# Optimization experiments

Hardware: AMD Instinct MI355X
Metric: run time of the kernel (lower is better)

## Reference

```python
import jax, jax.numpy as jnp
import numpy as np


def setup_inputs() -> dict:
    key = jax.random.key(0)
    k0, k1, k2, k3, k4 = jax.random.split(key, 5)
    Ns, N, D = 1024, 192, 24
    # spins in {-1, +1}
    x = (2.0 * jax.random.randint(k0, (Ns, N), 0, 2) - 1.0).astype(jnp.float32)
    # symmetric distance-index matrix with values in [0, D)
    r = jax.random.randint(k1, (N, N), 0, D)
    nd = jnp.minimum(r, r.T).astype(jnp.int32)
    W2 = 0.1 * jax.random.normal(k2, (D,), dtype=jnp.float32)
    W3 = 0.01 * jax.random.normal(k3, (D, D), dtype=jnp.float32)
    # positive mean-field coefficients so log(phi) is real
    phi = 0.5 + jax.random.uniform(k4, (N, 2), dtype=jnp.float32)
    return {"x": x, "W2": W2, "W3": W3, "phi": phi, "neighbors_distances": nd}


def reference(x, W2, W3, phi, neighbors_distances):
    # x: (Ns, N) spins in {-1,+1}; W2: (D,); W3: (D,D); phi: (N,2); nd: (N,N) int in [0,D)
    nd = neighbors_distances
    N = x.shape[-1]

    # J2[n] = 0.5 * sum_{i,j} x[n,i] * W2[nd[i,j]] * x[n,j]
    J2 = 0.5 * jnp.einsum('ni,ij,nj->n', x, W2[nd], x)

    # J3[n] = sum_{i,j,k} W3[nd[k,j], nd[i,j]] x[n,k] x[n,i] x[n,j]
    G = W3[nd]                                  # (N,N,D): G[k,j,d] = W3[nd[k,j], d]
    S = jnp.einsum('nk,kjd->njd', x, G)         # (Ns,N,D)
    j_idx = jnp.broadcast_to(jnp.arange(N)[None, :], (N, N))
    M = S[:, j_idx, nd]                         # (Ns,N,N): M[n,i,j] = S[n, j, nd[i,j]]
    J3 = jnp.einsum('nij,ni,nj->n', M, x, x)

    # mean-field: sum_i log(phi[i, (1+x[n,i])/2])
    idx = jax.lax.stop_gradient(((1.0 + x) * 0.5)).astype(jnp.int32)  # (Ns,N) in {0,1}
    mf = phi[jnp.arange(N)[None, :], idx]       # (Ns,N)
    logmf = jnp.sum(jnp.log(mf), axis=-1)

    return J2 + J3 + logmf
```

## Files before the change

kernel.cpp:

```cpp
#include <hip/hip_runtime.h>
#include <math.h>


#define NS   1024
#define NN   192
#define DD   24
#define CPAD 25

__global__ __launch_bounds__(NN) void jmf3_kernel(
    const float* __restrict__ x,
    const float* __restrict__ W2,
    const float* __restrict__ W3,
    const float* __restrict__ phi,
    const int*   __restrict__ nd,
    float* __restrict__ out)
{
    __shared__ float sx[NN];
    __shared__ float sW3[DD * DD];
    __shared__ float sW2[DD];
    __shared__ float sc[NN * CPAD];
    __shared__ float red[3];

    const int tid = threadIdx.x;
    const int n   = blockIdx.x;

    sx[tid] = x[n * NN + tid];
    sW3[tid]       = W3[tid];
    sW3[tid + 192] = W3[tid + 192];
    sW3[tid + 384] = W3[tid + 384];
    if (tid < DD) sW2[tid] = W2[tid];
    #pragma unroll
    for (int r = 0; r < CPAD; ++r) sc[tid * CPAD + r] = 0.0f;
    __syncthreads();

    const int j = tid;
    float* cj = &sc[j * CPAD];
    for (int i = 0; i < NN; ++i) {
        int r = nd[i * NN + j];
        cj[r] += sx[i];
    }

    float c[DD];
    #pragma unroll
    for (int r = 0; r < DD; ++r) c[r] = cj[r];

    float q = 0.0f, l2 = 0.0f;
    #pragma unroll
    for (int r = 0; r < DD; ++r) {
        float t = 0.0f;
        #pragma unroll
        for (int s = 0; s < DD; ++s) t = fmaf(sW3[r * DD + s], c[s], t);
        q  = fmaf(c[r], t, q);
        l2 = fmaf(sW2[r], c[r], l2);
    }

    const float xj  = sx[j];
    const int   idx = (xj > 0.0f) ? 1 : 0;
    float contrib = xj * (0.5f * l2 + q) + logf(phi[j * 2 + idx]);

    #pragma unroll
    for (int off = 32; off >= 1; off >>= 1)
        contrib += __shfl_down(contrib, off, 64);
    const int wave = tid >> 6;
    if ((tid & 63) == 0) red[wave] = contrib;
    __syncthreads();
    if (tid == 0) out[n] = red[0] + red[1] + red[2];
}

extern "C" void kernel_launch(void* const* d_in, const int* in_sizes, int n_in,
                              void* d_out, int out_size, void* d_ws, size_t ws_size,
                              hipStream_t stream) {
    const float* x   = (const float*)d_in[0];
    const float* W2  = (const float*)d_in[1];
    const float* W3  = (const float*)d_in[2];
    const float* phi = (const float*)d_in[3];
    const int*   nd  = (const int*)d_in[4];
    float* out = (float*)d_out;

    const int ns = in_sizes[0] / NN;
    jmf3_kernel<<<ns, NN, 0, stream>>>(x, W2, W3, phi, nd, out);
}
```

Measured before the change: 25.70 us.

## Replace per-sample scatter-add with bitmask popcount counts across two kernels

Splits the computation into a prep kernel and a main kernel. The prep kernel packs one-hot masks of the distance matrix per (j, r) and the sign bits of each sample with ballots, and also writes the mean-field log term. The main kernel computes each count c[r] as 2*popcount(mask & signs) - popcount(mask), parallelised over (sample, j), and accumulates results with atomic adds. This removes the serial 192-step LDS scatter loop and the repeated reads of nd, at the cost of a second launch, workspace traffic and float atomics, which make the summation order nondeterministic.

Measured after the change: 28.07 us. +9.3%, slower.

```diff
diff --git a/kernel.cpp b/kernel.cpp
--- a/kernel.cpp
+++ b/kernel.cpp
@@ -2,69 +2,114 @@
 #include <math.h>
 
 
-#define NS   1024
-#define NN   192
-#define DD   24
-#define CPAD 25
+#define NS 1024
+#define NN 192
+#define DD 24
 
-__global__ __launch_bounds__(NN) void jmf3_kernel(
+typedef unsigned long long ull;
+
+#define M_WORDS (NN * DD * 8)
+
+__global__ __launch_bounds__(192) void prep_kernel(
     const float* __restrict__ x,
+    const float* __restrict__ phi,
+    const int*   __restrict__ nd,
+    unsigned* __restrict__ Mbuf,
+    unsigned* __restrict__ Pd,
+    float* __restrict__ out)
+{
+    const int tid = threadIdx.x;
+    const int wv  = tid >> 6;
+    const int b   = blockIdx.x;
+
+    if (b < NN) {
+        const int j   = b;
+        const int ndv = nd[j * NN + tid];
+        #pragma unroll
+        for (int r = 0; r < DD; ++r) {
+            ull m = __ballot(ndv == r);
+            if ((tid & 63) == 0) {
+                unsigned* dst = &Mbuf[(j * DD + r) * 8 + 2 * wv];
+                dst[0] = (unsigned)m;
+                dst[1] = (unsigned)(m >> 32);
+            }
+        }
+    } else {
+        const int n   = b - NN;
+        const float xv = x[n * NN + tid];
+        const int bit  = (xv > 0.0f) ? 1 : 0;
+        ull m = __ballot(bit);
+        if ((tid & 63) == 0) {
+            Pd[(2 * wv    ) * NS + n] = (unsigned)m;
+            Pd[(2 * wv + 1) * NS + n] = (unsigned)(m >> 32);
+        }
+        float contrib = logf(phi[tid * 2 + bit]);
+        __shared__ float red[3];
+        #pragma unroll
+        for (int off = 32; off >= 1; off >>= 1)
+            contrib += __shfl_down(contrib, off, 64);
+        if ((tid & 63) == 0) red[wv] = contrib;
+        __syncthreads();
+        if (tid == 0) out[n] = red[0] + red[1] + red[2];
+    }
+}
+
+__global__ __launch_bounds__(256) void main_kernel(
     const float* __restrict__ W2,
     const float* __restrict__ W3,
-    const float* __restrict__ phi,
-    const int*   __restrict__ nd,
+    const unsigned* __restrict__ Mbuf,
+    const unsigned* __restrict__ Pd,
     float* __restrict__ out)
 {
-    __shared__ float sx[NN];
-    __shared__ float sW3[DD * DD];
-    __shared__ float sW2[DD];
-    __shared__ float sc[NN * CPAD];
-    __shared__ float red[3];
+    const int lane = threadIdx.x & 63;
+    const int wv   = threadIdx.x >> 6;
+    const int n    = blockIdx.x * 64 + lane;
+    int j = blockIdx.y * 4 + wv;
+    j = __builtin_amdgcn_readfirstlane(j);
 
-    const int tid = threadIdx.x;
-    const int n   = blockIdx.x;
+    const unsigned p0 = Pd[0 * NS + n];
+    const unsigned p1 = Pd[1 * NS + n];
+    const unsigned p2 = Pd[2 * NS + n];
+    const unsigned p3 = Pd[3 * NS + n];
+    const unsigned p4 = Pd[4 * NS + n];
+    const unsigned p5 = Pd[5 * NS + n];
 
-    sx[tid] = x[n * NN + tid];
-    sW3[tid]       = W3[tid];
-    sW3[tid + 192] = W3[tid + 192];
-    sW3[tid + 384] = W3[tid + 384];
-    if (tid < DD) sW2[tid] = W2[tid];
-    #pragma unroll
-    for (int r = 0; r < CPAD; ++r) sc[tid * CPAD + r] = 0.0f;
-    __syncthreads();
-
-    const int j = tid;
-    float* cj = &sc[j * CPAD];
-    for (int i = 0; i < NN; ++i) {
-        int r = nd[i * NN + j];
-        cj[r] += sx[i];
-    }
+    const unsigned* __restrict__ Mj = &Mbuf[j * DD * 8];
 
     float c[DD];
     #pragma unroll
-    for (int r = 0; r < DD; ++r) c[r] = cj[r];
+    for (int r = 0; r < DD; ++r) {
+        const unsigned m0 = Mj[r * 8 + 0];
+        const unsigned m1 = Mj[r * 8 + 1];
+        const unsigned m2 = Mj[r * 8 + 2];
+        const unsigned m3 = Mj[r * 8 + 3];
+        const unsigned m4 = Mj[r * 8 + 4];
+        const unsigned m5 = Mj[r * 8 + 5];
+        int pc = __popc(m0 & p0) + __popc(m1 & p1) + __popc(m2 & p2)
+               + __popc(m3 & p3) + __popc(m4 & p4) + __popc(m5 & p5);
+        int cnt = __popcll(((ull)m1 << 32) | m0)
+                + __popcll(((ull)m3 << 32) | m2)
+                + __popcll(((ull)m5 << 32) | m4);
+        c[r] = fmaf(2.0f, (float)pc, -(float)cnt);
+    }
 
     float q = 0.0f, l2 = 0.0f;
     #pragma unroll
     for (int r = 0; r < DD; ++r) {
         float t = 0.0f;
         #pragma unroll
-        for (int s = 0; s < DD; ++s) t = fmaf(sW3[r * DD + s], c[s], t);
+        for (int s = 0; s < DD; ++s) t = fmaf(W3[r * DD + s], c[s], t);
         q  = fmaf(c[r], t, q);
-        l2 = fmaf(sW2[r], c[r], l2);
+        l2 = fmaf(W2[r], c[r], l2);
     }
 
-    const float xj  = sx[j];
-    const int   idx = (xj > 0.0f) ? 1 : 0;
-    float contrib = xj * (0.5f * l2 + q) + logf(phi[j * 2 + idx]);
+    const int w = j >> 5, bpos = j & 31;
+    unsigned pw = (w == 0) ? p0 : (w == 1) ? p1 : (w == 2) ? p2
+                : (w == 3) ? p3 : (w == 4) ? p4 : p5;
+    const float xj = ((pw >> bpos) & 1u) ? 1.0f : -1.0f;
 
-    #pragma unroll
-    for (int off = 32; off >= 1; off >>= 1)
-        contrib += __shfl_down(contrib, off, 64);
-    const int wave = tid >> 6;
-    if ((tid & 63) == 0) red[wave] = contrib;
-    __syncthreads();
-    if (tid == 0) out[n] = red[0] + red[1] + red[2];
+    const float contrib = xj * fmaf(0.5f, l2, q);
+    unsafeAtomicAdd(&out[n], contrib);
 }
 
 extern "C" void kernel_launch(void* const* d_in, const int* in_sizes, int n_in,
@@ -77,6 +122,9 @@
     const int*   nd  = (const int*)d_in[4];
     float* out = (float*)d_out;
 
-    const int ns = in_sizes[0] / NN;
-    jmf3_kernel<<<ns, NN, 0, stream>>>(x, W2, W3, phi, nd, out);
+    unsigned* Mbuf = (unsigned*)d_ws;
+    unsigned* Pd   = (unsigned*)d_ws + M_WORDS;
+
+    prep_kernel<<<NN + NS, 192, 0, stream>>>(x, phi, nd, Mbuf, Pd, out);
+    main_kernel<<<dim3(NS / 64, NN / 4), 256, 0, stream>>>(W2, W3, Mbuf, Pd, out);
 }
```

## Compute distance-bin counts via bitmask popcount and split work across samples and columns

Applied to the files above, without the earlier changes.

Replaces the per-sample serial gather-accumulate over 192 rows with a bit-packed approach. Spins and distance-bin membership are packed into ballot masks, and each count c[r] is obtained as 2*popcount(mask & spins) - count. The grid now tiles 64 samples by 8 columns per block, with partial sums combined through atomic adds into a zeroed output. This removes the long LDS read-modify-write loop. In exchange it adds a memset launch, atomics, and W3 reads from global or scalar memory instead of LDS.

After: 35.05 us. 36.4% more time.

```diff
diff --git a/kernel.cpp b/kernel.cpp
--- a/kernel.cpp
+++ b/kernel.cpp
@@ -2,12 +2,13 @@
 #include <math.h>
 
 
-#define NS   1024
-#define NN   192
-#define DD   24
-#define CPAD 25
+#define NS 1024
+#define NN 192
+#define DD 24
 
-__global__ __launch_bounds__(NN) void jmf3_kernel(
+typedef unsigned long long ull;
+
+__global__ __launch_bounds__(512) void fused_kernel(
     const float* __restrict__ x,
     const float* __restrict__ W2,
     const float* __restrict__ W3,
@@ -15,56 +16,101 @@
     const int*   __restrict__ nd,
     float* __restrict__ out)
 {
-    __shared__ float sx[NN];
-    __shared__ float sW3[DD * DD];
-    __shared__ float sW2[DD];
-    __shared__ float sc[NN * CPAD];
-    __shared__ float red[3];
+    const int tid  = threadIdx.x;
+    const int lane = tid & 63;
+    const int wv   = tid >> 6;
+    const int n0   = blockIdx.x * 64;
+    const int j    = blockIdx.y * 8 + wv;
 
-    const int tid = threadIdx.x;
-    const int n   = blockIdx.x;
+    __shared__ unsigned Pp[64][6];
+    __shared__ unsigned Msk[8][24][8];
+    __shared__ float    part[8][64];
 
-    sx[tid] = x[n * NN + tid];
-    sW3[tid]       = W3[tid];
-    sW3[tid + 192] = W3[tid + 192];
-    sW3[tid + 384] = W3[tid + 384];
-    if (tid < DD) sW2[tid] = W2[tid];
     #pragma unroll
-    for (int r = 0; r < CPAD; ++r) sc[tid * CPAD + r] = 0.0f;
+    for (int q = 0; q < 8; ++q) {
+        const int s = wv * 8 + q;
+        const float* xr = &x[(size_t)(n0 + s) * NN];
+        unsigned keep = 0;
+        #pragma unroll
+        for (int c = 0; c < 3; ++c) {
+            const float v = xr[c * 64 + lane];
+            const ull m = __ballot(v > 0.0f);
+            const unsigned lo = (unsigned)m, hi = (unsigned)(m >> 32);
+            if (lane == 2 * c)     keep = lo;
+            if (lane == 2 * c + 1) keep = hi;
+        }
+        if (lane < 6) Pp[s][lane] = keep;
+    }
+
+    {
+        const int* ndr = &nd[(size_t)j * NN];
+        #pragma unroll
+        for (int c = 0; c < 3; ++c) {
+            const int ndv = ndr[c * 64 + lane];
+            unsigned wlo = 0, whi = 0;
+            #pragma unroll
+            for (int r = 0; r < DD; ++r) {
+                const ull m = __ballot(ndv == r);
+                if (lane == r) { wlo = (unsigned)m; whi = (unsigned)(m >> 32); }
+            }
+            if (lane < DD) {
+                Msk[wv][lane][2 * c]     = wlo;
+                Msk[wv][lane][2 * c + 1] = whi;
+            }
+        }
+    }
     __syncthreads();
 
-    const int j = tid;
-    float* cj = &sc[j * CPAD];
-    for (int i = 0; i < NN; ++i) {
-        int r = nd[i * NN + j];
-        cj[r] += sx[i];
+    if (tid < 8 * DD) {
+        const int jl = tid / DD, r = tid % DD;
+        int cnt = 0;
+        #pragma unroll
+        for (int w = 0; w < 6; ++w) cnt += __popc(Msk[jl][r][w]);
+        Msk[jl][r][6] = __float_as_uint(-(float)cnt);
     }
+    __syncthreads();
+
+    const unsigned p0 = Pp[lane][0], p1 = Pp[lane][1], p2 = Pp[lane][2];
+    const unsigned p3 = Pp[lane][3], p4 = Pp[lane][4], p5 = Pp[lane][5];
 
     float c[DD];
     #pragma unroll
-    for (int r = 0; r < DD; ++r) c[r] = cj[r];
+    for (int r = 0; r < DD; ++r) {
+        const unsigned m0 = Msk[wv][r][0], m1 = Msk[wv][r][1], m2 = Msk[wv][r][2];
+        const unsigned m3 = Msk[wv][r][3], m4 = Msk[wv][r][4], m5 = Msk[wv][r][5];
+        const float ncnt  = __uint_as_float(Msk[wv][r][6]);
+        const int pc = __popc(m0 & p0) + __popc(m1 & p1) + __popc(m2 & p2)
+                     + __popc(m3 & p3) + __popc(m4 & p4) + __popc(m5 & p5);
+        c[r] = fmaf(2.0f, (float)pc, ncnt);
+    }
 
     float q = 0.0f, l2 = 0.0f;
     #pragma unroll
     for (int r = 0; r < DD; ++r) {
         float t = 0.0f;
         #pragma unroll
-        for (int s = 0; s < DD; ++s) t = fmaf(sW3[r * DD + s], c[s], t);
+        for (int s = 0; s < DD; ++s) t = fmaf(W3[r * DD + s], c[s], t);
         q  = fmaf(c[r], t, q);
-        l2 = fmaf(sW2[r], c[r], l2);
+        l2 = fmaf(W2[r], c[r], l2);
     }
 
-    const float xj  = sx[j];
-    const int   idx = (xj > 0.0f) ? 1 : 0;
-    float contrib = xj * (0.5f * l2 + q) + logf(phi[j * 2 + idx]);
+    const int w = j >> 5, bpos = j & 31;
+    unsigned pw = (w == 0) ? p0 : (w == 1) ? p1 : (w == 2) ? p2
+                : (w == 3) ? p3 : (w == 4) ? p4 : p5;
+    const int   pos = (int)((pw >> bpos) & 1u);
+    const float xj  = pos ? 1.0f : -1.0f;
+    const float lp0 = logf(phi[j * 2 + 0]);
+    const float lp1 = logf(phi[j * 2 + 1]);
 
-    #pragma unroll
-    for (int off = 32; off >= 1; off >>= 1)
-        contrib += __shfl_down(contrib, off, 64);
-    const int wave = tid >> 6;
-    if ((tid & 63) == 0) red[wave] = contrib;
+    const float acc = xj * fmaf(0.5f, l2, q) + (pos ? lp1 : lp0);
+
+    part[wv][lane] = acc;
     __syncthreads();
-    if (tid == 0) out[n] = red[0] + red[1] + red[2];
+    if (wv == 0) {
+        float s = part[0][lane] + part[1][lane] + part[2][lane] + part[3][lane]
+                + part[4][lane] + part[5][lane] + part[6][lane] + part[7][lane];
+        unsafeAtomicAdd(&out[n0 + lane], s);
+    }
 }
 
 extern "C" void kernel_launch(void* const* d_in, const int* in_sizes, int n_in,
@@ -78,5 +124,6 @@
     float* out = (float*)d_out;
 
     const int ns = in_sizes[0] / NN;
-    jmf3_kernel<<<ns, NN, 0, stream>>>(x, W2, W3, phi, nd, out);
+    hipMemsetAsync(out, 0, (size_t)ns * sizeof(float), stream);
+    fused_kernel<<<dim3(ns / 64, NN / 8), 512, 0, stream>>>(x, W2, W3, phi, nd, out);
 }
```
